# Performance work log

Hardware: AMD Instinct MI355X
Metric: run time of the kernel (lower is better)

Reference implementation:

```python
import jax, jax.numpy as jnp
import numpy as np

B, T, D, H = 16384, 80, 12, 128


def setup_inputs() -> dict:
    key = jax.random.key(0)
    ks = jax.random.split(key, 20)
    stdv = lambda n: 1.0 / np.sqrt(n)
    u = lambda k, shp, s: jax.random.uniform(k, shp, jnp.float32, -s, s)
    inp = {
        'values': jax.random.normal(ks[0], (B, T, D), jnp.float32),
        'masks': (jax.random.uniform(ks[1], (B, T, D)) < 0.8).astype(jnp.float32),
        'deltas': jax.random.uniform(ks[2], (B, T, D), jnp.float32, 0.0, 5.0),
        'td_h_W': u(ks[3], (H, D), stdv(H)), 'td_h_b': u(ks[4], (H,), stdv(H)),
        'td_x_W': u(ks[5], (D, D), stdv(D)), 'td_x_b': u(ks[6], (D,), stdv(D)),
        'hist_W': u(ks[7], (D, H), stdv(H)), 'hist_b': u(ks[8], (D,), stdv(H)),
        'feat_W': u(ks[9], (D, D), stdv(D)), 'feat_b': u(ks[10], (D,), stdv(D)),
        'wc_W': u(ks[11], (D, 2 * D), stdv(2 * D)), 'wc_b': u(ks[12], (D,), stdv(2 * D)),
        'W_ih': u(ks[13], (4 * H, 2 * D), stdv(H)), 'b_ih': u(ks[14], (4 * H,), stdv(H)),
        'W_hh': u(ks[15], (4 * H, H), stdv(H)), 'b_hh': u(ks[16], (4 * H,), stdv(H)),
        'out_W': u(ks[17], (1, H), stdv(H)), 'out_b': u(ks[18], (1,), stdv(H)),
    }
    return inp


def _forward(values, masks, deltas, td_h_W, td_h_b, td_x_W, td_x_b,
             hist_W, hist_b, feat_W, feat_b, wc_W, wc_b,
             W_ih, b_ih, W_hh, b_hh, out_W, out_b):
    eye = jnp.eye(D, dtype=values.dtype)
    td_x_Wd = td_x_W * eye            # diagonal temporal decay
    feat_Wm = feat_W * (1.0 - eye)

    xs = (jnp.swapaxes(values, 0, 1),  # [T,B,D]
          jnp.swapaxes(masks, 0, 1),
          jnp.swapaxes(deltas, 0, 1))

    def step(carry, xmd):
        h, c, x_loss = carry
        x, m, d = xmd
        gamma_h = jnp.exp(-jax.nn.relu(d @ td_h_W.T + td_h_b))   # [B,H]
        gamma_x = jnp.exp(-jax.nn.relu(d @ td_x_Wd.T + td_x_b))  # [B,D]
        h = h * gamma_h
        x_h = h @ hist_W.T + hist_b
        denom = jnp.sum(m) + 1e-5
        x_loss += jnp.sum(jnp.abs(x - x_h) * m) / denom
        x_c = m * x + (1.0 - m) * x_h
        z_h = x_c @ feat_Wm.T + feat_b
        x_loss += jnp.sum(jnp.abs(x - z_h) * m) / denom
        alpha = jnp.concatenate([gamma_x, m], axis=1) @ wc_W.T + wc_b
        c_h = alpha * z_h + (1.0 - alpha) * x_h
        x_loss += jnp.sum(jnp.abs(x - c_h) * m) / denom
        c_c = m * x + (1.0 - m) * c_h
        inp = jnp.concatenate([c_c, m], axis=1)                  # [B,2D]
        gates = inp @ W_ih.T + b_ih + h @ W_hh.T + b_hh          # [B,4H]
        i, f, g, o = jnp.split(gates, 4, axis=1)
        c = jax.nn.sigmoid(f) * c + jax.nn.sigmoid(i) * jnp.tanh(g)
        h = jax.nn.sigmoid(o) * jnp.tanh(c)
        return (h, c, x_loss), c_c

    h0 = jnp.zeros((values.shape[0], H), values.dtype)
    c0 = jnp.zeros((values.shape[0], H), values.dtype)
    (h, c, x_loss), imps = jax.lax.scan(step, (h0, c0, jnp.float32(0.0)), xs)
    loss = x_loss / T
    predictions = jax.nn.sigmoid(h @ out_W.T + out_b)            # [B,1]
    imputations = jnp.swapaxes(imps, 0, 1)                       # [B,T,D]
    return loss, predictions, imputations


def reference(values, masks, deltas, td_h_W, td_h_b, td_x_W, td_x_b,
              hist_W, hist_b, feat_W, feat_b, wc_W, wc_b,
              W_ih, b_ih, W_hh, b_hh, out_W, out_b):
    return _forward(values, masks, deltas, td_h_W, td_h_b, td_x_W, td_x_b,
                    hist_W, hist_b, feat_W, feat_b, wc_W, wc_b,
                    W_ih, b_ih, W_hh, b_hh, out_W, out_b)
```

## Files before the change

kernel.cpp:

```cpp
#include <hip/hip_runtime.h>

#define B_ 16384
#define T_ 80
#define D_ 12
#define H_ 128
#define BT 32
#define NTH 512
#define NBLK (B_ / BT)

typedef unsigned short us_t;
typedef unsigned int u32_t;
typedef short bf16x8 __attribute__((ext_vector_type(8)));
typedef float f32x4 __attribute__((ext_vector_type(4)));

__device__ __forceinline__ us_t f2bf(float f){
  u32_t x = __float_as_uint(f);
  return (us_t)((x + 0x7FFFu + ((x >> 16) & 1u)) >> 16);
}
__device__ __forceinline__ float bf2f(us_t u){
  union { u32_t i; float f; } v; v.i = ((u32_t)u) << 16; return v.f;
}
__device__ __forceinline__ float rcpf(float x){ return __builtin_amdgcn_rcpf(x); }
__device__ __forceinline__ float sigm(float x){ return rcpf(1.f + __expf(-x)); }
__device__ __forceinline__ float tanhf_fast(float x){ return 1.f - 2.f * rcpf(1.f + __expf(2.f * x)); }

__global__ void k_denom(const float* __restrict__ masks, float* __restrict__ denomInv) {
  int t = blockIdx.x, tid = threadIdx.x;
  float s = 0.f;
  for (int b = tid; b < B_; b += 256) {
    const float4* p = (const float4*)(masks + ((size_t)b * T_ + t) * D_);
    float4 a = p[0], c = p[1], d = p[2];
    s += a.x + a.y + a.z + a.w + c.x + c.y + c.z + c.w + d.x + d.y + d.z + d.w;
  }
  __shared__ float r[256];
  r[tid] = s; __syncthreads();
  for (int st = 128; st > 0; st >>= 1) { if (tid < st) r[tid] += r[tid + st]; __syncthreads(); }
  if (tid == 0) denomInv[t] = 1.f / (r[0] + 1e-5f);
}

__global__ void k_pack(const float* __restrict__ W_ih, const float* __restrict__ W_hh,
                       const float* __restrict__ hist_W, const float* __restrict__ td_h_W,
                       const float* __restrict__ b_ih, const float* __restrict__ b_hh,
                       us_t* __restrict__ Wb, us_t* __restrict__ histB,
                       us_t* __restrict__ tdhwB, float* __restrict__ bias_pk) {
  int idx = blockIdx.x * 256 + threadIdx.x;
  if (idx < 81920) {
    int i = idx & 7, lane = (idx >> 3) & 63, rest = idx >> 9;
    int kc = rest % 5; rest /= 5;
    int g = rest & 3, w = rest >> 2;
    int n = g * 128 + w * 16 + (lane & 15);
    int k = kc * 32 + ((lane >> 4) << 3) + i;
    float v = 0.f;
    if (k < 24) v = W_ih[n * 24 + k];
    else if (k < 152) v = W_hh[n * 128 + (k - 24)];
    Wb[idx] = f2bf(v);
  } else if (idx < 83968) {
    int e = idx - 81920;
    int i = e & 7, lane = (e >> 3) & 63, kc = e >> 9;
    int col = lane & 15, k = kc * 32 + ((lane >> 4) << 3) + i;
    histB[e] = f2bf(col < 12 ? hist_W[col * 128 + k] : 0.f);
  } else if (idx < 88064) {
    int e = idx - 83968;
    int i = e & 7, lane = (e >> 3) & 63, w = e >> 9;
    int n = w * 16 + (lane & 15), k = ((lane >> 4) << 3) + i;
    tdhwB[e] = f2bf(k < 12 ? td_h_W[n * 12 + k] : 0.f);
  } else if (idx < 88576) {
    int e = idx - 88064;
    bias_pk[e] = b_ih[e] + b_hh[e];
  }
}

#define STAGE_WRITE(BUF, V) do { \
  if (la == 0) { \
    x_s[BUF][lb][lq*4+0] = (V).x; x_s[BUF][lb][lq*4+1] = (V).y; \
    x_s[BUF][lb][lq*4+2] = (V).z; x_s[BUF][lb][lq*4+3] = (V).w; \
  } else if (la == 1) { \
    m_s[BUF][lb][lq*4+0] = (V).x; m_s[BUF][lb][lq*4+1] = (V).y; \
    m_s[BUF][lb][lq*4+2] = (V).z; m_s[BUF][lb][lq*4+3] = (V).w; \
    float _mv0=(V).x,_mv1=(V).y,_mv2=(V).z,_mv3=(V).w; \
    int _k = 12 + lq*4; \
    A_s[BUF][(_k+0)>>3][lb][(_k+0)&7] = f2bf(_mv0); \
    A_s[BUF][(_k+1)>>3][lb][(_k+1)&7] = f2bf(_mv1); \
    A_s[BUF][(_k+2)>>3][lb][(_k+2)&7] = f2bf(_mv2); \
    A_s[BUF][(_k+3)>>3][lb][(_k+3)&7] = f2bf(_mv3); \
  } else { \
    float _dv[4] = {(V).x,(V).y,(V).z,(V).w}; \
    _Pragma("unroll") \
    for (int _j = 0; _j < 4; ++_j) { \
      int _i = lq*4+_j; \
      gx_s[BUF][lb][_i] = __expf(-fmaxf(fmaf(_dv[_j], tdxd_s[_i], tdxb_s[_i]), 0.f)); \
      dA_s[_i>>3][lb][_i&7] = f2bf(_dv[_j]); \
    } \
  } \
} while(0)

__global__ __launch_bounds__(NTH) void k_main(
    const float* __restrict__ values, const float* __restrict__ masks, const float* __restrict__ deltas,
    const float* __restrict__ td_h_b, const float* __restrict__ td_x_W, const float* __restrict__ td_x_b,
    const float* __restrict__ hist_b, const float* __restrict__ feat_W, const float* __restrict__ feat_b,
    const float* __restrict__ wc_W, const float* __restrict__ wc_b,
    const float* __restrict__ out_W, const float* __restrict__ out_b,
    const float* __restrict__ denomInv, const float* __restrict__ bias_pk,
    const us_t* __restrict__ Wb, const us_t* __restrict__ histB, const us_t* __restrict__ tdhwB,
    float* __restrict__ blockLoss, float* __restrict__ out_pred, float* __restrict__ out_imp) {

  __shared__ __align__(16) us_t A_s[2][20][BT][8];
  __shared__ __align__(16) us_t dA_s[4][BT][8];
  __shared__ __align__(16) us_t histB_s[4][64][8];
  __shared__ float x_s[2][BT][13], m_s[2][BT][13], gx_s[2][BT][13];
  __shared__ float cct_s[BT][13], xh_s[BT][13];
  __shared__ float featW_s[12][12], wcW_s[12][24];
  __shared__ float featb_s[12], wcb_s[12], tdxd_s[12], tdxb_s[12];
  __shared__ float outW_s[128];
  __shared__ float outb_s;
  __shared__ float red_s[NTH];

  const int tid = threadIdx.x;
  const int bs = blockIdx.x * BT;
  const int w = tid >> 6, l = tid & 63;
  const int lr = l & 15, lg = l >> 4;

  for (int i = tid; i < 144; i += NTH)
    featW_s[i / 12][i % 12] = ((i / 12) == (i % 12)) ? 0.f : feat_W[i];
  for (int i = tid; i < 288; i += NTH) ((float*)wcW_s)[i] = wc_W[i];
  if (tid < 12) {
    featb_s[tid] = feat_b[tid]; wcb_s[tid] = wc_b[tid];
    tdxd_s[tid] = td_x_W[tid * 12 + tid]; tdxb_s[tid] = td_x_b[tid];
  }
  if (tid < 128) outW_s[tid] = out_W[tid];
  if (tid == 0) outb_s = out_b[0];
  for (int i = tid; i < 2 * 20 * BT * 8; i += NTH) ((us_t*)A_s)[i] = 0;
  for (int i = tid; i < 4 * BT * 8; i += NTH) ((us_t*)dA_s)[i] = 0;
  for (int i = tid; i < 2048; i += NTH) ((us_t*)histB_s)[i] = histB[i];

  bf16x8 bq[4][5];
  #pragma unroll
  for (int g = 0; g < 4; ++g)
    #pragma unroll
    for (int kc = 0; kc < 5; ++kc)
      bq[g][kc] = *(const bf16x8*)(Wb + (size_t)((((w * 4 + g) * 5 + kc) * 64 + l) << 3));
  const bf16x8 twf = *(const bf16x8*)(tdhwB + (size_t)(((w * 64) + l) << 3));
  float bj[4];
  #pragma unroll
  for (int g = 0; g < 4; ++g) bj[g] = bias_pk[g * 128 + w * 16 + lr];
  const float tdhb_j = td_h_b[w * 16 + lr];
  const float hbias = hist_b[lr < 12 ? lr : 0];

  const int lt = tid - 128;
  const bool isLoader = (lt >= 0 && lt < 288);
  const int la = isLoader ? lt / 96 : 0;
  const int lrm = isLoader ? lt % 96 : 0;
  const int lb = lrm / 3, lq = lrm % 3;
  const float* lsrc = (la == 0) ? values : (la == 1) ? masks : deltas;

  float c_st[2][4] = {{0.f,0.f,0.f,0.f},{0.f,0.f,0.f,0.f}};
  float lossAcc = 0.f;
  int cur = 0;
  __syncthreads();

  if (isLoader) {
    float4 pv = *(const float4*)(lsrc + ((size_t)(bs + lb) * T_) * D_ + lq * 4);
    STAGE_WRITE(0, pv);
  }
  __syncthreads();

  for (int t = 0; t < T_; ++t) {
    const float dInv = denomInv[t];
    const int nxt = cur ^ 1;
    float4 ldv;

    if (w < 2) {
      f32x4 xacc = {0.f, 0.f, 0.f, 0.f};
      #pragma unroll
      for (int kc = 0; kc < 4; ++kc) {
        const bf16x8 af = *(const bf16x8*)&A_s[cur][3 + kc * 4 + lg][w * 16 + lr][0];
        const bf16x8 hf = *(const bf16x8*)&histB_s[kc][l][0];
        xacc = __builtin_amdgcn_mfma_f32_16x16x32_bf16(af, hf, xacc, 0, 0, 0);
      }
      if (lr < 12) {
        #pragma unroll
        for (int r = 0; r < 4; ++r) xh_s[w * 16 + lg * 4 + r][lr] = xacc[r] + hbias;
      }
    } else if (isLoader) {
      if (t + 1 < T_)
        ldv = *(const float4*)(lsrc + ((size_t)(bs + lb) * T_ + (t + 1)) * D_ + lq * 4);
    } else if (t > 0) {
      int ib = (tid - 416) / 3, iq = (tid - 416) % 3;
      float4 v = make_float4(cct_s[ib][iq * 4 + 0], cct_s[ib][iq * 4 + 1],
                             cct_s[ib][iq * 4 + 2], cct_s[ib][iq * 4 + 3]);
      *(float4*)(out_imp + ((size_t)(bs + ib) * T_ + (t - 1)) * D_ + iq * 4) = v;
    }
    __syncthreads();

    if (isLoader && (t + 1 < T_)) STAGE_WRITE(nxt, ldv);
    if (tid < 384) {
      int b = tid & 31, i = tid >> 5;
      float xh = xh_s[b][i], xv = x_s[cur][b][i], mv = m_s[cur][b][i];
      lossAcc = fmaf(fabsf(xv - xh) * mv, dInv, lossAcc);
      float zh = featb_s[i];
      #pragma unroll
      for (int k = 0; k < 12; ++k) {
        float xck = fmaf(m_s[cur][b][k], x_s[cur][b][k] - xh_s[b][k], xh_s[b][k]);
        zh = fmaf(xck, featW_s[i][k], zh);
      }
      lossAcc = fmaf(fabsf(xv - zh) * mv, dInv, lossAcc);
      float al = wcb_s[i];
      #pragma unroll
      for (int k = 0; k < 12; ++k) {
        al = fmaf(gx_s[cur][b][k], wcW_s[i][k], al);
        al = fmaf(m_s[cur][b][k], wcW_s[i][12 + k], al);
      }
      float ch = fmaf(al, zh - xh, xh);
      lossAcc = fmaf(fabsf(xv - ch) * mv, dInv, lossAcc);
      float cc = fmaf(mv, xv - ch, ch);
      cct_s[b][i] = cc;
      A_s[cur][i >> 3][b][i & 7] = f2bf(cc);
    }
    __syncthreads();

    {
      f32x4 acc[2][4];
      #pragma unroll
      for (int m = 0; m < 2; ++m)
        #pragma unroll
        for (int g = 0; g < 4; ++g) acc[m][g] = (f32x4){0.f, 0.f, 0.f, 0.f};
      #pragma unroll
      for (int kc = 0; kc < 5; ++kc) {
        const bf16x8 a0 = *(const bf16x8*)&A_s[cur][kc * 4 + lg][lr][0];
        const bf16x8 a1 = *(const bf16x8*)&A_s[cur][kc * 4 + lg][16 + lr][0];
        #pragma unroll
        for (int g = 0; g < 4; ++g) {
          acc[0][g] = __builtin_amdgcn_mfma_f32_16x16x32_bf16(a0, bq[g][kc], acc[0][g], 0, 0, 0);
          acc[1][g] = __builtin_amdgcn_mfma_f32_16x16x32_bf16(a1, bq[g][kc], acc[1][g], 0, 0, 0);
        }
      }
      f32x4 g0 = {0.f,0.f,0.f,0.f}, g1 = {0.f,0.f,0.f,0.f};
      const bf16x8 d0 = *(const bf16x8*)&dA_s[lg][lr][0];
      const bf16x8 d1 = *(const bf16x8*)&dA_s[lg][16 + lr][0];
      g0 = __builtin_amdgcn_mfma_f32_16x16x32_bf16(d0, twf, g0, 0, 0, 0);
      g1 = __builtin_amdgcn_mfma_f32_16x16x32_bf16(d1, twf, g1, 0, 0, 0);
      const bool dec = (t + 1 < T_);
      const int kgh = 3 + 2 * w + (lr >> 3), pgh = lr & 7;
      #pragma unroll
      for (int m = 0; m < 2; ++m) {
        #pragma unroll
        for (int r = 0; r < 4; ++r) {
          float gi = sigm(acc[m][0][r] + bj[0]);
          float gf = sigm(acc[m][1][r] + bj[1]);
          float gg = tanhf_fast(acc[m][2][r] + bj[2]);
          float go = sigm(acc[m][3][r] + bj[3]);
          float c = fmaf(gf, c_st[m][r], gi * gg);
          c_st[m][r] = c;
          float hn = go * tanhf_fast(c);
          float pre = (m == 0 ? g0[r] : g1[r]) + tdhb_j;
          float gh = dec ? __expf(-fmaxf(pre, 0.f)) : 1.f;
          A_s[nxt][kgh][m * 16 + lg * 4 + r][pgh] = f2bf(hn * gh);
        }
      }
    }
    __syncthreads();
    cur = nxt;
  }

  if (tid >= 416) {
    int ib = (tid - 416) / 3, iq = (tid - 416) % 3;
    float4 v = make_float4(cct_s[ib][iq * 4 + 0], cct_s[ib][iq * 4 + 1],
                           cct_s[ib][iq * 4 + 2], cct_s[ib][iq * 4 + 3]);
    *(float4*)(out_imp + ((size_t)(bs + ib) * T_ + (T_ - 1)) * D_ + iq * 4) = v;
  }

  if (tid < BT) {
    float a = outb_s;
    #pragma unroll 4
    for (int k = 0; k < H_; ++k)
      a = fmaf(bf2f(A_s[cur][3 + (k >> 3)][tid][k & 7]), outW_s[k], a);
    out_pred[bs + tid] = sigm(a);
  }

  red_s[tid] = lossAcc;
  __syncthreads();
  for (int s = NTH / 2; s > 0; s >>= 1) { if (tid < s) red_s[tid] += red_s[tid + s]; __syncthreads(); }
  if (tid == 0) blockLoss[blockIdx.x] = red_s[0];
}

__global__ void k_final(const float* __restrict__ blockLoss, float* __restrict__ out_loss) {
  __shared__ float r[256];
  int tid = threadIdx.x;
  r[tid] = blockLoss[tid] + blockLoss[tid + 256];
  __syncthreads();
  for (int s = 128; s > 0; s >>= 1) { if (tid < s) r[tid] += r[tid + s]; __syncthreads(); }
  if (tid == 0) out_loss[0] = r[0] * (1.f / (float)T_);
}

extern "C" void kernel_launch(void* const* d_in, const int* in_sizes, int n_in,
                              void* d_out, int out_size, void* d_ws, size_t ws_size,
                              hipStream_t stream) {
  const float* values = (const float*)d_in[0];
  const float* masks  = (const float*)d_in[1];
  const float* deltas = (const float*)d_in[2];
  const float* td_h_W = (const float*)d_in[3];
  const float* td_h_b = (const float*)d_in[4];
  const float* td_x_W = (const float*)d_in[5];
  const float* td_x_b = (const float*)d_in[6];
  const float* hist_W = (const float*)d_in[7];
  const float* hist_b = (const float*)d_in[8];
  const float* feat_W = (const float*)d_in[9];
  const float* feat_b = (const float*)d_in[10];
  const float* wc_W   = (const float*)d_in[11];
  const float* wc_b   = (const float*)d_in[12];
  const float* W_ih   = (const float*)d_in[13];
  const float* b_ih   = (const float*)d_in[14];
  const float* W_hh   = (const float*)d_in[15];
  const float* b_hh   = (const float*)d_in[16];
  const float* out_W  = (const float*)d_in[17];
  const float* out_b  = (const float*)d_in[18];

  float* ws_f      = (float*)d_ws;
  float* denomInv  = ws_f;
  float* bias_pk   = ws_f + 128;
  float* blockLoss = ws_f + 1024;
  us_t* Wb    = (us_t*)(ws_f + 2048);
  us_t* histB = Wb + 81920;
  us_t* tdhwB = histB + 2048;

  float* out_f = (float*)d_out;

  k_denom<<<T_, 256, 0, stream>>>(masks, denomInv);
  k_pack<<<346, 256, 0, stream>>>(W_ih, W_hh, hist_W, td_h_W, b_ih, b_hh,
                                  Wb, histB, tdhwB, bias_pk);
  k_main<<<NBLK, NTH, 0, stream>>>(values, masks, deltas, td_h_b, td_x_W, td_x_b,
                                   hist_b, feat_W, feat_b, wc_W, wc_b,
                                   out_W, out_b, denomInv, bias_pk, Wb, histB, tdhwB,
                                   blockLoss, out_f + 1, out_f + 1 + B_);
  k_final<<<1, 256, 0, stream>>>(blockLoss, out_f);
}
```

Before: 530.4 us.

## Prescale gate weights by log2e, fold biases into MFMA accumulators, offload alpha

Gate, bias and time-decay weights are prescaled by -log2(e) (or 2·log2(e) for the tanh gate), so the activations use exp2 directly with no extra multiply. Biases are loaded into the MFMA accumulator init instead of being added afterwards. The alpha combination is moved to the otherwise idle loader/writer threads in the first phase, which shortens the 384-thread imputation phase, and the three loss terms are summed before a single scale. Bias and weights now pass through bf16 rounding after scaling, which may shift numerics slightly.

```diff
diff --git a/kernel.cpp b/kernel.cpp
--- a/kernel.cpp
+++ b/kernel.cpp
@@ -8,6 +8,9 @@
 #define NTH 512
 #define NBLK (B_ / BT)
 
+#define NLOG2E -1.4426950408889634f
+#define TWOLOG2E 2.8853900817779268f
+
 typedef unsigned short us_t;
 typedef unsigned int u32_t;
 typedef short bf16x8 __attribute__((ext_vector_type(8)));
@@ -21,8 +24,12 @@
   union { u32_t i; float f; } v; v.i = ((u32_t)u) << 16; return v.f;
 }
 __device__ __forceinline__ float rcpf(float x){ return __builtin_amdgcn_rcpf(x); }
+#if __has_builtin(__builtin_amdgcn_exp2f)
+__device__ __forceinline__ float exp2f_(float x){ return __builtin_amdgcn_exp2f(x); }
+#else
+__device__ __forceinline__ float exp2f_(float x){ return __expf(0.6931471805599453f * x); }
+#endif
 __device__ __forceinline__ float sigm(float x){ return rcpf(1.f + __expf(-x)); }
-__device__ __forceinline__ float tanhf_fast(float x){ return 1.f - 2.f * rcpf(1.f + __expf(2.f * x)); }
 
 __global__ void k_denom(const float* __restrict__ masks, float* __restrict__ denomInv) {
   int t = blockIdx.x, tid = threadIdx.x;
@@ -53,7 +60,8 @@
     float v = 0.f;
     if (k < 24) v = W_ih[n * 24 + k];
     else if (k < 152) v = W_hh[n * 128 + (k - 24)];
-    Wb[idx] = f2bf(v);
+    float s = (g == 2) ? TWOLOG2E : NLOG2E;
+    Wb[idx] = f2bf(v * s);
   } else if (idx < 83968) {
     int e = idx - 81920;
     int i = e & 7, lane = (e >> 3) & 63, kc = e >> 9;
@@ -63,10 +71,12 @@
     int e = idx - 83968;
     int i = e & 7, lane = (e >> 3) & 63, w = e >> 9;
     int n = w * 16 + (lane & 15), k = ((lane >> 4) << 3) + i;
-    tdhwB[e] = f2bf(k < 12 ? td_h_W[n * 12 + k] : 0.f);
+    tdhwB[e] = f2bf(k < 12 ? td_h_W[n * 12 + k] * NLOG2E : 0.f);
   } else if (idx < 88576) {
     int e = idx - 88064;
-    bias_pk[e] = b_ih[e] + b_hh[e];
+    int g = e >> 7;
+    float s = (g == 2) ? TWOLOG2E : NLOG2E;
+    bias_pk[e] = (b_ih[e] + b_hh[e]) * s;
   }
 }
 
@@ -88,7 +98,7 @@
     _Pragma("unroll") \
     for (int _j = 0; _j < 4; ++_j) { \
       int _i = lq*4+_j; \
-      gx_s[BUF][lb][_i] = __expf(-fmaxf(fmaf(_dv[_j], tdxd_s[_i], tdxb_s[_i]), 0.f)); \
+      gx_s[BUF][lb][_i] = exp2f_(fminf(fmaf(_dv[_j], tdxd_s[_i], tdxb_s[_i]), 0.f)); \
       dA_s[_i>>3][lb][_i&7] = f2bf(_dv[_j]); \
     } \
   } \
@@ -108,7 +118,7 @@
   __shared__ __align__(16) us_t dA_s[4][BT][8];
   __shared__ __align__(16) us_t histB_s[4][64][8];
   __shared__ float x_s[2][BT][13], m_s[2][BT][13], gx_s[2][BT][13];
-  __shared__ float cct_s[BT][13], xh_s[BT][13];
+  __shared__ float cct_s[BT][13], xh_s[BT][13], al_s[BT][13];
   __shared__ float featW_s[12][12], wcW_s[12][24];
   __shared__ float featb_s[12], wcb_s[12], tdxd_s[12], tdxb_s[12];
   __shared__ float outW_s[128];
@@ -125,7 +135,8 @@
   for (int i = tid; i < 288; i += NTH) ((float*)wcW_s)[i] = wc_W[i];
   if (tid < 12) {
     featb_s[tid] = feat_b[tid]; wcb_s[tid] = wc_b[tid];
-    tdxd_s[tid] = td_x_W[tid * 12 + tid]; tdxb_s[tid] = td_x_b[tid];
+    tdxd_s[tid] = td_x_W[tid * 12 + tid] * NLOG2E;
+    tdxb_s[tid] = td_x_b[tid] * NLOG2E;
   }
   if (tid < 128) outW_s[tid] = out_W[tid];
   if (tid == 0) outb_s = out_b[0];
@@ -140,10 +151,10 @@
     for (int kc = 0; kc < 5; ++kc)
       bq[g][kc] = *(const bf16x8*)(Wb + (size_t)((((w * 4 + g) * 5 + kc) * 64 + l) << 3));
   const bf16x8 twf = *(const bf16x8*)(tdhwB + (size_t)(((w * 64) + l) << 3));
-  float bj[4];
+  float bjs[4];
   #pragma unroll
-  for (int g = 0; g < 4; ++g) bj[g] = bias_pk[g * 128 + w * 16 + lr];
-  const float tdhb_j = td_h_b[w * 16 + lr];
+  for (int g = 0; g < 4; ++g) bjs[g] = bias_pk[g * 128 + w * 16 + lr];
+  const float tdhb_j = td_h_b[w * 16 + lr] * NLOG2E;
   const float hbias = hist_b[lr < 12 ? lr : 0];
 
   const int lt = tid - 128;
@@ -181,14 +192,24 @@
         #pragma unroll
         for (int r = 0; r < 4; ++r) xh_s[w * 16 + lg * 4 + r][lr] = xacc[r] + hbias;
       }
-    } else if (isLoader) {
-      if (t + 1 < T_)
-        ldv = *(const float4*)(lsrc + ((size_t)(bs + lb) * T_ + (t + 1)) * D_ + lq * 4);
-    } else if (t > 0) {
-      int ib = (tid - 416) / 3, iq = (tid - 416) % 3;
-      float4 v = make_float4(cct_s[ib][iq * 4 + 0], cct_s[ib][iq * 4 + 1],
-                             cct_s[ib][iq * 4 + 2], cct_s[ib][iq * 4 + 3]);
-      *(float4*)(out_imp + ((size_t)(bs + ib) * T_ + (t - 1)) * D_ + iq * 4) = v;
+    } else {
+      if (isLoader) {
+        if (t + 1 < T_)
+          ldv = *(const float4*)(lsrc + ((size_t)(bs + lb) * T_ + (t + 1)) * D_ + lq * 4);
+      } else if (t > 0) {
+        int ib = (tid - 416) / 3, iq = (tid - 416) % 3;
+        float4 v = make_float4(cct_s[ib][iq * 4 + 0], cct_s[ib][iq * 4 + 1],
+                               cct_s[ib][iq * 4 + 2], cct_s[ib][iq * 4 + 3]);
+        *(float4*)(out_imp + ((size_t)(bs + ib) * T_ + (t - 1)) * D_ + iq * 4) = v;
+      }
+      int ai = tid - 128, b = ai & 31, i = ai >> 5;
+      float al = wcb_s[i];
+      #pragma unroll
+      for (int k = 0; k < 12; ++k) {
+        al = fmaf(gx_s[cur][b][k], wcW_s[i][k], al);
+        al = fmaf(m_s[cur][b][k], wcW_s[i][12 + k], al);
+      }
+      al_s[b][i] = al;
     }
     __syncthreads();
 
@@ -196,22 +217,18 @@
     if (tid < 384) {
       int b = tid & 31, i = tid >> 5;
       float xh = xh_s[b][i], xv = x_s[cur][b][i], mv = m_s[cur][b][i];
-      lossAcc = fmaf(fabsf(xv - xh) * mv, dInv, lossAcc);
+      float es = fabsf(xv - xh) * mv;
       float zh = featb_s[i];
       #pragma unroll
       for (int k = 0; k < 12; ++k) {
         float xck = fmaf(m_s[cur][b][k], x_s[cur][b][k] - xh_s[b][k], xh_s[b][k]);
         zh = fmaf(xck, featW_s[i][k], zh);
       }
-      lossAcc = fmaf(fabsf(xv - zh) * mv, dInv, lossAcc);
-      float al = wcb_s[i];
-      #pragma unroll
-      for (int k = 0; k < 12; ++k) {
-        al = fmaf(gx_s[cur][b][k], wcW_s[i][k], al);
-        al = fmaf(m_s[cur][b][k], wcW_s[i][12 + k], al);
-      }
+      es += fabsf(xv - zh) * mv;
+      float al = al_s[b][i];
       float ch = fmaf(al, zh - xh, xh);
-      lossAcc = fmaf(fabsf(xv - ch) * mv, dInv, lossAcc);
+      es += fabsf(xv - ch) * mv;
+      lossAcc = fmaf(es, dInv, lossAcc);
       float cc = fmaf(mv, xv - ch, ch);
       cct_s[b][i] = cc;
       A_s[cur][i >> 3][b][i & 7] = f2bf(cc);
@@ -223,7 +240,8 @@
       #pragma unroll
       for (int m = 0; m < 2; ++m)
         #pragma unroll
-        for (int g = 0; g < 4; ++g) acc[m][g] = (f32x4){0.f, 0.f, 0.f, 0.f};
+        for (int g = 0; g < 4; ++g)
+          acc[m][g] = (f32x4){bjs[g], bjs[g], bjs[g], bjs[g]};
       #pragma unroll
       for (int kc = 0; kc < 5; ++kc) {
         const bf16x8 a0 = *(const bf16x8*)&A_s[cur][kc * 4 + lg][lr][0];
@@ -234,7 +252,8 @@
           acc[1][g] = __builtin_amdgcn_mfma_f32_16x16x32_bf16(a1, bq[g][kc], acc[1][g], 0, 0, 0);
         }
       }
-      f32x4 g0 = {0.f,0.f,0.f,0.f}, g1 = {0.f,0.f,0.f,0.f};
+      f32x4 g0 = {tdhb_j, tdhb_j, tdhb_j, tdhb_j};
+      f32x4 g1 = g0;
       const bf16x8 d0 = *(const bf16x8*)&dA_s[lg][lr][0];
       const bf16x8 d1 = *(const bf16x8*)&dA_s[lg][16 + lr][0];
       g0 = __builtin_amdgcn_mfma_f32_16x16x32_bf16(d0, twf, g0, 0, 0, 0);
@@ -245,16 +264,16 @@
       for (int m = 0; m < 2; ++m) {
         #pragma unroll
         for (int r = 0; r < 4; ++r) {
-          float gi = sigm(acc[m][0][r] + bj[0]);
-          float gf = sigm(acc[m][1][r] + bj[1]);
-          float gg = tanhf_fast(acc[m][2][r] + bj[2]);
-          float go = sigm(acc[m][3][r] + bj[3]);
+          float gi = rcpf(1.f + exp2f_(acc[m][0][r]));
+          float gf = rcpf(1.f + exp2f_(acc[m][1][r]));
+          float gg = 1.f - 2.f * rcpf(1.f + exp2f_(acc[m][2][r]));
+          float go = rcpf(1.f + exp2f_(acc[m][3][r]));
           float c = fmaf(gf, c_st[m][r], gi * gg);
           c_st[m][r] = c;
-          float hn = go * tanhf_fast(c);
-          float pre = (m == 0 ? g0[r] : g1[r]) + tdhb_j;
-          float gh = dec ? __expf(-fmaxf(pre, 0.f)) : 1.f;
-          A_s[nxt][kgh][m * 16 + lg * 4 + r][pgh] = f2bf(hn * gh);
+          float th = 1.f - 2.f * rcpf(1.f + exp2f_(TWOLOG2E * c));
+          float pre = (m == 0 ? g0[r] : g1[r]);
+          float gh = dec ? exp2f_(fminf(pre, 0.f)) : 1.f;
+          A_s[nxt][kgh][m * 16 + lg * 4 + r][pgh] = f2bf(go * th * gh);
         }
       }
     }
```

New measurement: 492.2 us. 7.2% less time.
